# Kernel tuning notes

Measured on AMD Instinct MI355X. Metric: run time of the kernel, lower is better.

The kernel has to match this reference:

```python
import jax, jax.numpy as jnp
import numpy as np

N = 50000
E = 800000
IN_DIM = 128
HID = 64
HEADS = 4

def _gat_layer(h, src, dst, W, al, ar, Wres, activation):
    # h: [N, F_in]; W: [F_in, HEADS*HID]; al/ar: [HEADS, HID]
    n = h.shape[0]
    ft = (h @ W).reshape(n, HEADS, HID)                    # [N,H,D]
    el = (ft * al).sum(-1)                                  # [N,H]
    er = (ft * ar).sum(-1)                                  # [N,H]
    e = jax.nn.leaky_relu(el[src] + er[dst], 0.2)           # [E,H]
    m = jax.ops.segment_max(e, dst, num_segments=n)         # per-dst max for stable softmax
    ex = jnp.exp(e - m[dst])
    den = jax.ops.segment_sum(ex, dst, num_segments=n)
    alpha = ex / den[dst]                                   # edge softmax [E,H]
    out = jax.ops.segment_sum(alpha[:, :, None] * ft[src], dst, num_segments=n)  # [N,H,D]
    res = (h @ Wres).reshape(n, HEADS, HID) if Wres is not None else h.reshape(n, HEADS, HID)
    out = out + res
    return activation(out) if activation is not None else out


def setup_inputs() -> dict:
    key = jax.random.key(0)
    ks = jax.random.split(key, 16)
    def lin(k, fi, fo):
        return jax.random.normal(k, (fi, fo), jnp.float32) / np.sqrt(fi)
    HD = HEADS * HID
    inp = {
        "h": jax.random.normal(ks[0], (N, IN_DIM), jnp.float32),
        "src": jax.random.randint(ks[1], (E,), 0, N, jnp.int32),
        "dst": jax.random.randint(ks[2], (E,), 0, N, jnp.int32),
        "W1": lin(ks[3], IN_DIM, HD),
        "Wr1": lin(ks[4], IN_DIM, HD),
        "al1": jax.random.normal(ks[5], (HEADS, HID), jnp.float32) * 0.1,
        "ar1": jax.random.normal(ks[6], (HEADS, HID), jnp.float32) * 0.1,
        "W2": lin(ks[7], HD, HD),
        "al2": jax.random.normal(ks[8], (HEADS, HID), jnp.float32) * 0.1,
        "ar2": jax.random.normal(ks[9], (HEADS, HID), jnp.float32) * 0.1,
        "W3": lin(ks[10], HD, HD),
        "al3": jax.random.normal(ks[11], (HEADS, HID), jnp.float32) * 0.1,
        "ar3": jax.random.normal(ks[12], (HEADS, HID), jnp.float32) * 0.1,
        "Wm1": lin(ks[13], HID, HID),
        "bm1": jnp.zeros((HID,), jnp.float32),
        "Wm2": lin(ks[14], HID, 1),
        "bm2": jnp.zeros((1,), jnp.float32),
    }
    return inp


def reference(h, src, dst, W1, Wr1, al1, ar1, W2, al2, ar2, W3, al3, ar3, Wm1, bm1, Wm2, bm2):
    x = _gat_layer(h, src, dst, W1, al1, ar1, Wr1, jax.nn.relu)   # [N,H,D]
    x = x.reshape(x.shape[0], -1)                                  # [N,H*D]
    x = _gat_layer(x, src, dst, W2, al2, ar2, None, jax.nn.relu)  # identity residual (in==H*D)
    x = x.reshape(x.shape[0], -1)
    x = _gat_layer(x, src, dst, W3, al3, ar3, None, None)
    hf = x.mean(1)                                                 # [N,HID]
    diff = jnp.abs(hf[src] - hf[dst])                              # [E,HID]
    z = jax.nn.relu(diff @ Wm1 + bm1)
    score = jax.nn.sigmoid(z @ Wm2 + bm2).squeeze(-1)              # [E]
    return score
```

## Files before the change

### kernel.cpp

```cpp
#include <hip/hip_runtime.h>
#include <hip/hip_bf16.h>

typedef unsigned short u16;
typedef unsigned char u8;
typedef __attribute__((ext_vector_type(8))) short bf16x8;
typedef __attribute__((ext_vector_type(4))) float f32x4;
typedef __attribute__((ext_vector_type(2))) float f32x2;

__device__ __forceinline__ float bf2f(u16 u){
  union { unsigned int i; float f; } v; v.i = ((unsigned int)u) << 16; return v.f;
}
__device__ __forceinline__ u16 f2bf(float f){
  union { float f; unsigned int i; } v; v.f = f;
  unsigned int lsb = (v.i >> 16) & 1u;
  v.i += 0x7fffu + lsb;
  return (u16)(v.i >> 16);
}
__device__ __forceinline__ unsigned pkbf(float a, float b){
  __hip_bfloat162 h = __float22bfloat162_rn(make_float2(a, b));
  union { __hip_bfloat162 h2; unsigned u; } c; c.h2 = h; return c.u;
}
__device__ __forceinline__ u8 f2fp8(float f){
  int p = __builtin_amdgcn_cvt_pk_fp8_f32(f, f, 0, false);
  return (u8)(p & 0xFF);
}

__global__ void k_sniff(const u16* __restrict__ p, int* __restrict__ flag){
  __shared__ int s[256];
  int tid = threadIdx.x;
  u16 v = p[2 * tid];
  int e = (v >> 7) & 0xFF;
  s[tid] = (e >= 100 && e <= 135) ? 1 : 0;
  __syncthreads();
  for (int off = 128; off; off >>= 1){
    if (tid < off) s[tid] += s[tid + off];
    __syncthreads();
  }
  if (tid == 0) *flag = (s[0] < 180) ? 1 : 0;
}

struct PrepEnt { const void* s; void* d; void* d2; int n; int K; int mode; int bstart; };
struct Prep16 { PrepEnt e[16]; };
__global__ void k_prep(Prep16 tab, const u16* __restrict__ hsrc){
  __shared__ int s[256];
  __shared__ u16 tl[32][33];
  {
    int tid = threadIdx.x;
    u16 v = hsrc[2 * tid];
    int e = (v >> 7) & 0xFF;
    s[tid] = (e >= 100 && e <= 135) ? 1 : 0;
    __syncthreads();
    for (int off = 128; off; off >>= 1){
      if (tid < off) s[tid] += s[tid + off];
      __syncthreads();
    }
  }
  const int flag = (s[0] < 180) ? 1 : 0;
  __syncthreads();

  const int bx = blockIdx.x;
  int y = 0;
  #pragma unroll
  for (int i = 1; i < 16; ++i) if (bx >= tab.e[i].bstart) y = i;
  PrepEnt en = tab.e[y];
  const int nblk = ((y < 15) ? tab.e[y + 1].bstart : (int)gridDim.x) - en.bstart;
  const int lb = bx - en.bstart;
  const int T = nblk * 256;
  const int t0 = lb * 256 + threadIdx.x;

  if (en.mode == 1){
    u16* d = (u16*)en.d;
    for (int i = t0; i < en.n; i += T){
      u16 o[4];
      if (flag){
        float4 v = ((const float4*)en.s)[i];
        o[0] = f2bf(v.x); o[1] = f2bf(v.y); o[2] = f2bf(v.z); o[3] = f2bf(v.w);
      } else {
        uint2 v = ((const uint2*)en.s)[i];
        o[0] = (u16)v.x; o[1] = (u16)(v.x >> 16); o[2] = (u16)v.y; o[3] = (u16)(v.y >> 16);
      }
      uint2 w; w.x = o[0] | ((unsigned)o[1] << 16); w.y = o[2] | ((unsigned)o[3] << 16);
      ((uint2*)d)[i] = w;
    }
  } else if (en.mode == 0){
    u16* d = (u16*)en.d;
    for (int i = t0; i < en.n; i += T){
      if (flag) d[i] = f2bf(((const float*)en.s)[i]);
      else      d[i] = ((const u16*)en.s)[i];
    }
  } else if (en.mode == 2){
    u16* wt = (u16*)en.d;
    const int K = en.K;
    const int tk = lb >> 3, tc = lb & 7;
    const int tx = threadIdx.x & 31, ty = threadIdx.x >> 5;
    #pragma unroll
    for (int r = 0; r < 4; ++r){
      int row = tk * 32 + ty + r * 8, col = tc * 32 + tx;
      u16 b;
      if (flag) b = f2bf(((const float*)en.s)[row * 256 + col]);
      else      b = ((const u16*)en.s)[row * 256 + col];
      tl[ty + r * 8][tx] = b;
    }
    __syncthreads();
    #pragma unroll
    for (int r = 0; r < 4; ++r){
      int c = tc * 32 + ty + r * 8, k = tk * 32 + tx;
      wt[(size_t)c * K + k] = tl[tx][ty + r * 8];
    }
  } else {
    const int* dstp = (const int*)en.s;
    int* slotp = (int*)en.d;
    int* cur   = (int*)en.d2;
    for (int base = t0; base < en.n; base += 4 * T){
      int e0 = base, e1 = base + T, e2 = base + 2 * T, e3 = base + 3 * T;
      bool v0 = e0 < en.n, v1 = e1 < en.n, v2 = e2 < en.n, v3 = e3 < en.n;
      int d0 = 0, d1 = 0, d2 = 0, d3 = 0;
      if (v0) d0 = dstp[e0];
      if (v1) d1 = dstp[e1];
      if (v2) d2 = dstp[e2];
      if (v3) d3 = dstp[e3];
      int p0 = 0, p1 = 0, p2 = 0, p3 = 0;
      if (v0) p0 = atomicAdd(&cur[d0], 1);
      if (v1) p1 = atomicAdd(&cur[d1], 1);
      if (v2) p2 = atomicAdd(&cur[d2], 1);
      if (v3) p3 = atomicAdd(&cur[d3], 1);
      if (v0) slotp[e0] = p0;
      if (v1) slotp[e1] = p1;
      if (v2) slotp[e2] = p2;
      if (v3) slotp[e3] = p3;
    }
  }
}

__global__ void k_scan1(const int* __restrict__ cnt, int* __restrict__ rowptr,
                        int* __restrict__ bsums, int N){
  __shared__ int s[256];
  int i = blockIdx.x * 256 + threadIdx.x;
  int v = (i < N) ? cnt[i] : 0;
  s[threadIdx.x] = v; __syncthreads();
  for (int off = 1; off < 256; off <<= 1){
    int x = 0;
    if (threadIdx.x >= off) x = s[threadIdx.x - off];
    __syncthreads();
    s[threadIdx.x] += x;
    __syncthreads();
  }
  if (i < N) rowptr[i + 1] = s[threadIdx.x];
  if (threadIdx.x == 255) bsums[blockIdx.x] = s[255];
}
__global__ void k_scan2(int* __restrict__ bsums, int nb){
  __shared__ int s[256];
  int t = threadIdx.x;
  int v = (t < nb) ? bsums[t] : 0;
  s[t] = v; __syncthreads();
  for (int off = 1; off < 256; off <<= 1){
    int x = 0;
    if (t >= off) x = s[t - off];
    __syncthreads();
    s[t] += x;
    __syncthreads();
  }
  if (t < nb) bsums[t] = s[t] - v;
}
__global__ void k_scan3(int* __restrict__ rowptr, const int* __restrict__ bsums, int N){
  int i = blockIdx.x * 256 + threadIdx.x;
  if (i < N){
    rowptr[i + 1] += bsums[blockIdx.x];
    if (i == 0) rowptr[0] = 0;
  }
}
__global__ void k_place(const int* __restrict__ src, const int* __restrict__ dst,
                        const int* __restrict__ slot, const int* __restrict__ rowptr,
                        int4* __restrict__ csrp, int E){
  const int T = gridDim.x * 256;
  for (int i = blockIdx.x * 256 + threadIdx.x; i < E; i += T){
    int d = dst[i];
    csrp[rowptr[d] + slot[i]] = make_int4(src[i], d, i, 0);
  }
}
__global__ void k_extract(const int4* __restrict__ csrp, int* __restrict__ csrs, int E){
  int i = blockIdx.x * 256 + threadIdx.x;
  if (i < E) csrs[i] = csrp[i].x;
}

__global__ __launch_bounds__(256, 4) void mfma_gemm_v4(
    const u16* __restrict__ X, const u16* __restrict__ WT, const u16* __restrict__ WTr,
    u8* __restrict__ FT8, u16* __restrict__ XA,
    const u16* __restrict__ al, const u16* __restrict__ ar,
    float* __restrict__ el4, float* __restrict__ er4, int N, int K)
{
  extern __shared__ u16 Bs[];
  const int wv = threadIdx.x >> 6;
  const int lane = threadIdx.x & 63;
  const int m = lane & 15;
  const int q = lane >> 4;
  const int row0 = blockIdx.x * 128 + wv * 32;
  const int col0 = blockIdx.y * 128;
  const u16* W = (blockIdx.z == 0) ? WT : WTr;

  {
    const int spr = K >> 3;
    const int ish = (spr == 32) ? 5 : 4;
    const int nIss = K >> 4;
    for (int j = 0; j < nIss; ++j){
      int cbase = (j * 4 + wv) * 64;
      int chunk = cbase + lane;
      int col = chunk >> ish;
      int slot = chunk & (spr - 1);
      int gslot = slot ^ (col & 7);
      const u16* srcp = W + (size_t)(col0 + col) * K + gslot * 8;
      u16* dstp = Bs + (size_t)cbase * 8;
      __builtin_amdgcn_global_load_lds((const unsigned int*)srcp,
                                       (unsigned int*)dstp, 16, 0, 0);
    }
  }

  f32x4 acc[2][8];
  #pragma unroll
  for (int g = 0; g < 2; ++g)
    #pragma unroll
    for (int t = 0; t < 8; ++t) acc[g][t] = (f32x4){0.f, 0.f, 0.f, 0.f};
  const int rA = row0 + m, rB = row0 + 16 + m;
  const bool vA = rA < N, vB = rB < N;
  const u16* apA = X + (size_t)rA * K + q * 8;
  const u16* apB = X + (size_t)rB * K + q * 8;

  asm volatile("s_waitcnt vmcnt(0)" ::: "memory");
  __syncthreads();

  const int mh = m & 7;
  for (int k0 = 0; k0 < K; k0 += 32){
    bf16x8 aA = {}, aB = {};
    if (vA) aA = *(const bf16x8*)(apA + k0);
    if (vB) aB = *(const bf16x8*)(apB + k0);
    const int sb = (k0 >> 3) + q;
    #pragma unroll
    for (int t = 0; t < 8; ++t){
      const u16* bp = Bs + (size_t)(t * 16 + m) * K + (size_t)(sb ^ mh) * 8;
      bf16x8 b = *(const bf16x8*)bp;
      acc[0][t] = __builtin_amdgcn_mfma_f32_16x16x32_bf16(aA, b, acc[0][t], 0, 0, 0);
      acc[1][t] = __builtin_amdgcn_mfma_f32_16x16x32_bf16(aB, b, acc[1][t], 0, 0, 0);
    }
  }

  if (blockIdx.z == 0){
    float alv[8], arv[8];
    #pragma unroll
    for (int t = 0; t < 8; ++t){
      alv[t] = bf2f(al[col0 + t * 16 + m]);
      arv[t] = bf2f(ar[col0 + t * 16 + m]);
    }
    #pragma unroll
    for (int g = 0; g < 2; ++g)
      #pragma unroll
      for (int r = 0; r < 4; ++r){
        float pe[2] = {0.f, 0.f}, pr[2] = {0.f, 0.f};
        #pragma unroll
        for (int t = 0; t < 8; ++t){
          pe[t >> 2] += acc[g][t][r] * alv[t];
          pr[t >> 2] += acc[g][t][r] * arv[t];
        }
        #pragma unroll
        for (int mk = 1; mk < 16; mk <<= 1){
          pe[0] += __shfl_xor(pe[0], mk); pe[1] += __shfl_xor(pe[1], mk);
          pr[0] += __shfl_xor(pr[0], mk); pr[1] += __shfl_xor(pr[1], mk);
        }
        int rr = row0 + g * 16 + q * 4 + r;
        if (m == 0 && rr < N){
          *(float2*)(el4 + (size_t)rr * 4 + blockIdx.y * 2) = make_float2(pe[0], pe[1]);
          *(float2*)(er4 + (size_t)rr * 4 + blockIdx.y * 2) = make_float2(pr[0], pr[1]);
        }
      }
    #pragma unroll
    for (int g = 0; g < 2; ++g)
      #pragma unroll
      for (int t = 0; t < 8; ++t){
        int col = col0 + t * 16 + m;
        #pragma unroll
        for (int r = 0; r < 4; ++r){
          int rr = row0 + g * 16 + q * 4 + r;
          if (rr < N) FT8[(size_t)rr * 256 + col] = f2fp8(acc[g][t][r]);
        }
      }
  } else {
    #pragma unroll
    for (int g = 0; g < 2; ++g)
      #pragma unroll
      for (int t = 0; t < 8; ++t){
        int col = col0 + t * 16 + m;
        #pragma unroll
        for (int r = 0; r < 4; ++r){
          int rr = row0 + g * 16 + q * 4 + r;
          if (rr < N) XA[(size_t)rr * 256 + col] = f2bf(acc[g][t][r]);
        }
      }
  }
}

__global__ __launch_bounds__(256) void aggregate7(
    const u8* __restrict__ ft8, const float* __restrict__ el4, const float* __restrict__ er4,
    const int* __restrict__ rowptr, const int* __restrict__ csrs,
    const u16* __restrict__ residb, u16* __restrict__ outb,
    u16* __restrict__ hf, int do_hf, int N)
{
  __shared__ float sal[4][64][4];
  __shared__ int   sof[4][64];
  const int w = threadIdx.x >> 6, lane = threadIdx.x & 63;
  const int d = blockIdx.x * 4 + w;
  if (d >= N) return;
  const int beg = rowptr[d], deg = rowptr[d + 1] - beg;
  const int H = lane >> 5;
  const int c = lane & 31;
  const int hg = c >> 3;
  f32x2 acc2[4];
  #pragma unroll
  for (int i = 0; i < 4; ++i) acc2[i] = (f32x2){0.f, 0.f};

  if (deg > 0){
    const float4 erd = ((const float4*)er4)[d];
    const int dc = min(deg, 64);
    float x0 = 0.f, x1 = 0.f, x2 = 0.f, x3 = 0.f; int sc = 0;
    float d0 = 0.f, d1 = 0.f, d2 = 0.f, d3 = 0.f;
    for (int j = lane; j < deg; j += 64){
      int s = csrs[beg + j];
      float4 ql = ((const float4*)el4)[s];
      float e0 = ql.x + erd.x; e0 = (e0 > 0.f) ? e0 : 0.2f * e0;
      float e1 = ql.y + erd.y; e1 = (e1 > 0.f) ? e1 : 0.2f * e1;
      float e2 = ql.z + erd.z; e2 = (e2 > 0.f) ? e2 : 0.2f * e2;
      float e3 = ql.w + erd.w; e3 = (e3 > 0.f) ? e3 : 0.2f * e3;
      float t0 = __expf(fminf(e0, 60.f)), t1 = __expf(fminf(e1, 60.f));
      float t2 = __expf(fminf(e2, 60.f)), t3 = __expf(fminf(e3, 60.f));
      if (j < 64){ x0 = t0; x1 = t1; x2 = t2; x3 = t3; sc = s; }
      d0 += t0; d1 += t1; d2 += t2; d3 += t3;
    }
    for (int mk = 1; mk < dc; mk <<= 1){
      d0 += __shfl_xor(d0, mk); d1 += __shfl_xor(d1, mk);
      d2 += __shfl_xor(d2, mk); d3 += __shfl_xor(d3, mk);
    }
    const float i0 = 1.f / d0, i1 = 1.f / d1, i2 = 1.f / d2, i3 = 1.f / d3;

    for (int c0 = 0; c0 < deg; c0 += 64){
      int cs = min(64, deg - c0);
      if (lane < cs){
        float t0, t1, t2, t3; int s;
        if (c0 == 0){ t0 = x0; t1 = x1; t2 = x2; t3 = x3; s = sc; }
        else {
          s = csrs[beg + c0 + lane];
          float4 ql = ((const float4*)el4)[s];
          float e0 = ql.x + erd.x; e0 = (e0 > 0.f) ? e0 : 0.2f * e0;
          float e1 = ql.y + erd.y; e1 = (e1 > 0.f) ? e1 : 0.2f * e1;
          float e2 = ql.z + erd.z; e2 = (e2 > 0.f) ? e2 : 0.2f * e2;
          float e3 = ql.w + erd.w; e3 = (e3 > 0.f) ? e3 : 0.2f * e3;
          t0 = __expf(fminf(e0, 60.f)); t1 = __expf(fminf(e1, 60.f));
          t2 = __expf(fminf(e2, 60.f)); t3 = __expf(fminf(e3, 60.f));
        }
        sal[w][lane][0] = t0 * i0; sal[w][lane][1] = t1 * i1;
        sal[w][lane][2] = t2 * i2; sal[w][lane][3] = t3 * i3;
        sof[w][lane] = s << 8;
      }
      __builtin_amdgcn_wave_barrier();
      for (int j0 = 0; j0 < cs; j0 += 4){
        int jA = j0 + H, jB = j0 + 2 + H;
        bool bA = jA < cs, bB = jB < cs;
        float aA = 0.f, aB = 0.f;
        int offA = 0, offB = 0;
        if (bA){ aA = sal[w][jA][hg]; offA = sof[w][jA]; }
        if (bB){ aB = sal[w][jB][hg]; offB = sof[w][jB]; }
        uint2 vA = {}, vB = {};
        if (bA) vA = *(const uint2*)(ft8 + (size_t)(unsigned)offA + c * 8);
        if (bB) vB = *(const uint2*)(ft8 + (size_t)(unsigned)offB + c * 8);
        if (bA){
          f32x2 a2 = (f32x2){aA, aA};
          acc2[0] += __builtin_amdgcn_cvt_pk_f32_fp8(vA.x, 0) * a2;
          acc2[1] += __builtin_amdgcn_cvt_pk_f32_fp8(vA.x, 1) * a2;
          acc2[2] += __builtin_amdgcn_cvt_pk_f32_fp8(vA.y, 0) * a2;
          acc2[3] += __builtin_amdgcn_cvt_pk_f32_fp8(vA.y, 1) * a2;
        }
        if (bB){
          f32x2 a2 = (f32x2){aB, aB};
          acc2[0] += __builtin_amdgcn_cvt_pk_f32_fp8(vB.x, 0) * a2;
          acc2[1] += __builtin_amdgcn_cvt_pk_f32_fp8(vB.x, 1) * a2;
          acc2[2] += __builtin_amdgcn_cvt_pk_f32_fp8(vB.y, 0) * a2;
          acc2[3] += __builtin_amdgcn_cvt_pk_f32_fp8(vB.y, 1) * a2;
        }
      }
      __builtin_amdgcn_wave_barrier();
    }
  }
  float acc[8];
  #pragma unroll
  for (int i = 0; i < 4; ++i){ acc[2 * i] = acc2[i].x; acc[2 * i + 1] = acc2[i].y; }
  #pragma unroll
  for (int i = 0; i < 8; ++i) acc[i] += __shfl_xor(acc[i], 32);
  uint4 rv = *(const uint4*)(residb + (size_t)d * 256 + c * 8);
  float rr[8];
  {
    union { unsigned u; float f; } t;
    t.u = rv.x << 16; rr[0] = t.f; t.u = rv.x & 0xffff0000u; rr[1] = t.f;
    t.u = rv.y << 16; rr[2] = t.f; t.u = rv.y & 0xffff0000u; rr[3] = t.f;
    t.u = rv.z << 16; rr[4] = t.f; t.u = rv.z & 0xffff0000u; rr[5] = t.f;
    t.u = rv.w << 16; rr[6] = t.f; t.u = rv.w & 0xffff0000u; rr[7] = t.f;
  }
  if (!do_hf){
    if (H == 0){
      float o[8];
      #pragma unroll
      for (int i = 0; i < 8; ++i) o[i] = fmaxf(acc[i] + rr[i], 0.f);
      uint4 ov;
      ov.x = pkbf(o[0], o[1]); ov.y = pkbf(o[2], o[3]);
      ov.z = pkbf(o[4], o[5]); ov.w = pkbf(o[6], o[7]);
      *(uint4*)(outb + (size_t)d * 256 + c * 8) = ov;
    }
  } else {
    #pragma unroll
    for (int i = 0; i < 8; ++i){
      float o = acc[i] + rr[i];
      o += __shfl_xor(o, 8);
      o += __shfl_xor(o, 16);
      acc[i] = 0.25f * o;
    }
    if (lane < 8){
      uint4 ov;
      ov.x = pkbf(acc[0], acc[1]); ov.y = pkbf(acc[2], acc[3]);
      ov.z = pkbf(acc[4], acc[5]); ov.w = pkbf(acc[6], acc[7]);
      *(uint4*)(hf + (size_t)d * 64 + lane * 8) = ov;
    }
  }
}

__global__ __launch_bounds__(256) void edge_mlp_csr(
    const u16* __restrict__ hfb, const int4* __restrict__ csrp,
    const u16* __restrict__ Wm1, const u16* __restrict__ bm1,
    const u16* __restrict__ Wm2, const u16* __restrict__ bm2,
    void* __restrict__ out, int E, const int* __restrict__ flag)
{
  const int lane = threadIdx.x & 63;
  const int m = lane & 15;
  const int q = lane >> 4;
  const int is_f32 = *flag;

  bf16x8 bfr[4][2];
  #pragma unroll
  for (int t = 0; t < 4; ++t)
    #pragma unroll
    for (int ks = 0; ks < 2; ++ks)
      #pragma unroll
      for (int j = 0; j < 8; ++j)
        bfr[t][ks][j] = (short)Wm1[(size_t)(ks * 32 + q * 8 + j) * 64 + t * 16 + m];

  float b1v[4], w2v[4];
  #pragma unroll
  for (int t = 0; t < 4; ++t){
    b1v[t] = bf2f(bm1[t * 16 + m]);
    w2v[t] = bf2f(Wm2[t * 16 + m]);
  }
  const float b2 = bf2f(bm2[0]);

  const int wid = blockIdx.x * 4 + (threadIdx.x >> 6);
  const int nw  = gridDim.x * 4;
  for (int e0 = wid * 16; e0 < E; e0 += nw * 16){
    int e = e0 + m; if (e >= E) e = E - 1;
    int4 ed = csrp[e];
    const u16* ps = hfb + (size_t)ed.x * 64;
    const u16* pd = hfb + (size_t)ed.y * 64;
    union { bf16x8 v; uint4 u; } af[2];
    #pragma unroll
    for (int ks = 0; ks < 2; ++ks){
      bf16x8 vs = *(const bf16x8*)(ps + ks * 32 + q * 8);
      bf16x8 vd = *(const bf16x8*)(pd + ks * 32 + q * 8);
      unsigned pk[4];
      #pragma unroll
      for (int pp = 0; pp < 4; ++pp){
        float a0 = fabsf(bf2f((u16)vs[2 * pp])     - bf2f((u16)vd[2 * pp]));
        float a1 = fabsf(bf2f((u16)vs[2 * pp + 1]) - bf2f((u16)vd[2 * pp + 1]));
        pk[pp] = pkbf(a0, a1);
      }
      af[ks].u = make_uint4(pk[0], pk[1], pk[2], pk[3]);
    }
    f32x4 acc[4];
    #pragma unroll
    for (int t = 0; t < 4; ++t) acc[t] = (f32x4){0.f, 0.f, 0.f, 0.f};
    #pragma unroll
    for (int ks = 0; ks < 2; ++ks)
      #pragma unroll
      for (int t = 0; t < 4; ++t)
        acc[t] = __builtin_amdgcn_mfma_f32_16x16x32_bf16(af[ks].v, bfr[t][ks], acc[t], 0, 0, 0);
    #pragma unroll
    for (int r = 0; r < 4; ++r){
      float p = 0.f;
      #pragma unroll
      for (int t = 0; t < 4; ++t)
        p += fmaxf(acc[t][r] + b1v[t], 0.f) * w2v[t];
      #pragma unroll
      for (int mm = 1; mm < 16; mm <<= 1) p += __shfl_xor(p, mm);
      int slot = e0 + q * 4 + r;
      if (m == 0 && slot < E){
        int eid = csrp[slot].z;
        float sc = 1.f / (1.f + __expf(-(p + b2)));
        if (is_f32) ((float*)out)[eid] = sc;
        else        ((u16*)out)[eid]   = f2bf(sc);
      }
    }
  }
}

extern "C" void kernel_launch(void* const* d_in, const int* in_sizes, int n_in,
                              void* d_out, int out_size, void* d_ws, size_t ws_size,
                              hipStream_t stream)
{
  const int* src = (const int*)d_in[1];
  const int* dst = (const int*)d_in[2];

  const int N = in_sizes[0] / 128;
  const int E = in_sizes[1];

  char* p = (char*)d_ws;
  auto alloc = [&](size_t bytes) -> char* {
    char* r = p; p += (bytes + 255) & ~(size_t)255; return r;
  };
  int* flag   = (int*)  alloc(4);
  u16* hc     = (u16*)  alloc((size_t)N * 128 * 2);
  u8*  FT8    = (u8*)   alloc((size_t)N * 256);
  u16* XA     = (u16*)  alloc((size_t)N * 256 * 2);
  u16* XB     = (u16*)  alloc((size_t)N * 256 * 2);
  float* el   = (float*)alloc((size_t)N * 4 * 4);
  float* er   = (float*)alloc((size_t)N * 4 * 4);
  u16* hfb    = (u16*)  alloc((size_t)N * 64 * 2);
  int* rowptr = (int*)  alloc((size_t)(N + 1) * 4);
  int* cursor = (int*)  alloc((size_t)N * 4);
  int* slot   = (int*)  alloc((size_t)E * 4);
  int4* csrp  = (int4*) alloc((size_t)E * 16);
  int* csrs   = (int*)  alloc((size_t)E * 4);
  int* bsums  = (int*)  alloc(1024);
  u16* WT1    = (u16*)  alloc(128 * 256 * 2);
  u16* WTr1   = (u16*)  alloc(128 * 256 * 2);
  u16* WT2    = (u16*)  alloc(256 * 256 * 2);
  u16* WT3    = (u16*)  alloc(256 * 256 * 2);
  u16* al1c   = (u16*)  alloc(256 * 2);
  u16* ar1c   = (u16*)  alloc(256 * 2);
  u16* al2c   = (u16*)  alloc(256 * 2);
  u16* ar2c   = (u16*)  alloc(256 * 2);
  u16* al3c   = (u16*)  alloc(256 * 2);
  u16* ar3c   = (u16*)  alloc(256 * 2);
  u16* Wm1c   = (u16*)  alloc(4096 * 2);
  u16* bm1c   = (u16*)  alloc(64 * 2);
  u16* Wm2c   = (u16*)  alloc(64 * 2);
  u16* bm2c   = (u16*)  alloc(2);

  const int nb = (N + 255) / 256;
  const int ge = (E + 255) / 256;
  const u16* hsrc = (const u16*)d_in[0];

  k_sniff<<<1, 256, 0, stream>>>(hsrc, flag);
  hipMemsetAsync(cursor, 0, (size_t)N * 4, stream);

  {
    Prep16 t{};
    int b = 0;
    auto put = [&](int idx, const void* s, void* d, void* d2, int n, int K,
                   int mode, int nblk){
      t.e[idx] = {s, d, d2, n, K, mode, b};
      b += nblk;
    };
    put(0,  dst,      slot,  cursor, E,         0,   4, 1024);
    put(1,  d_in[0],  hc,    nullptr, N * 32,   0,   1, 768);
    put(2,  d_in[3],  WT1,   nullptr, 0,        128, 2, 32);
    put(3,  d_in[4],  WTr1,  nullptr, 0,        128, 2, 32);
    put(4,  d_in[7],  WT2,   nullptr, 0,        256, 2, 64);
    put(5,  d_in[10], WT3,   nullptr, 0,        256, 2, 64);
    put(6,  d_in[5],  al1c,  nullptr, 256,      0,   0, 1);
    put(7,  d_in[6],  ar1c,  nullptr, 256,      0,   0, 1);
    put(8,  d_in[8],  al2c,  nullptr, 256,      0,   0, 1);
    put(9,  d_in[9],  ar2c,  nullptr, 256,      0,   0, 1);
    put(10, d_in[11], al3c,  nullptr, 256,      0,   0, 1);
    put(11, d_in[12], ar3c,  nullptr, 256,      0,   0, 1);
    put(12, d_in[13], Wm1c,  nullptr, 4096,     0,   0, 1);
    put(13, d_in[14], bm1c,  nullptr, 64,       0,   0, 1);
    put(14, d_in[15], Wm2c,  nullptr, 64,       0,   0, 1);
    put(15, d_in[16], bm2c,  nullptr, 1,        0,   0, 1);
    k_prep<<<dim3(b), 256, 0, stream>>>(t, hsrc);
  }

  k_scan1<<<nb, 256, 0, stream>>>(cursor, rowptr, bsums, N);
  k_scan2<<<1, 256, 0, stream>>>(bsums, nb);
  k_scan3<<<nb, 256, 0, stream>>>(rowptr, bsums, N);
  k_place<<<512, 256, 0, stream>>>(src, dst, slot, rowptr, csrp, E);
  k_extract<<<ge, 256, 0, stream>>>(csrp, csrs, E);

  const dim3 gA3((N + 127) / 128, 2);
  const dim3 gL1((N + 127) / 128, 2, 2);
  const int gG = (N + 3) / 4;
  const int lds1 = 128 * 128 * 2;
  const int lds2 = 128 * 256 * 2;
  mfma_gemm_v4<<<gL1, 256, lds1, stream>>>(hc, WT1, WTr1, FT8, XA, al1c, ar1c, el, er, N, 128);
  aggregate7<<<gG, 256, 0, stream>>>(FT8, el, er, rowptr, csrs, XA, XB, nullptr, 0, N);
  mfma_gemm_v4<<<gA3, 256, lds2, stream>>>(XB, WT2, WT2, FT8, XA, al2c, ar2c, el, er, N, 256);
  aggregate7<<<gG, 256, 0, stream>>>(FT8, el, er, rowptr, csrs, XB, XA, nullptr, 0, N);
  mfma_gemm_v4<<<gA3, 256, lds2, stream>>>(XA, WT3, WT3, FT8, XB, al3c, ar3c, el, er, N, 256);
  aggregate7<<<gG, 256, 0, stream>>>(FT8, el, er, rowptr, csrs, XA, nullptr, hfb, 1, N);
  edge_mlp_csr<<<2048, 256, 0, stream>>>(hfb, csrp, Wm1c, bm1c, Wm2c, bm2c,
                                         d_out, E, flag);
}
```

Measured before the change: 419.7 us.

## Process four destination nodes per wave with one-pass softmax in aggregation

```diff
diff --git a/kernel.cpp b/kernel.cpp
--- a/kernel.cpp
+++ b/kernel.cpp
@@ -297,133 +297,134 @@
   }
 }
 
-__global__ __launch_bounds__(256) void aggregate7(
+__global__ __launch_bounds__(256) void aggregate8(
     const u8* __restrict__ ft8, const float* __restrict__ el4, const float* __restrict__ er4,
     const int* __restrict__ rowptr, const int* __restrict__ csrs,
     const u16* __restrict__ residb, u16* __restrict__ outb,
     u16* __restrict__ hf, int do_hf, int N)
 {
-  __shared__ float sal[4][64][4];
-  __shared__ int   sof[4][64];
+  __shared__ float sal[4][4][17][4];
+  __shared__ int   sof[4][4][16];
   const int w = threadIdx.x >> 6, lane = threadIdx.x & 63;
-  const int d = blockIdx.x * 4 + w;
-  if (d >= N) return;
-  const int beg = rowptr[d], deg = rowptr[d + 1] - beg;
-  const int H = lane >> 5;
-  const int c = lane & 31;
-  const int hg = c >> 3;
-  f32x2 acc2[4];
+  const int g = lane >> 4, t = lane & 15;
+  const int hd = t >> 2;
+  const int d = blockIdx.x * 16 + w * 4 + g;
+  const bool vd = d < N;
+  int beg = 0, deg = 0;
+  if (vd){ beg = rowptr[d]; deg = rowptr[d + 1] - beg; }
+  int mdeg = deg;
+  mdeg = max(mdeg, __shfl_xor(mdeg, 16));
+  mdeg = max(mdeg, __shfl_xor(mdeg, 32));
+  float4 erd = make_float4(0.f, 0.f, 0.f, 0.f);
+  if (vd) erd = ((const float4*)er4)[d];
+
+  f32x2 acc2[8];
   #pragma unroll
-  for (int i = 0; i < 4; ++i) acc2[i] = (f32x2){0.f, 0.f};
-
-  if (deg > 0){
-    const float4 erd = ((const float4*)er4)[d];
-    const int dc = min(deg, 64);
-    float x0 = 0.f, x1 = 0.f, x2 = 0.f, x3 = 0.f; int sc = 0;
-    float d0 = 0.f, d1 = 0.f, d2 = 0.f, d3 = 0.f;
-    for (int j = lane; j < deg; j += 64){
-      int s = csrs[beg + j];
+  for (int i = 0; i < 8; ++i) acc2[i] = (f32x2){0.f, 0.f};
+  float den[4] = {0.f, 0.f, 0.f, 0.f};
+
+  for (int c0 = 0; c0 < mdeg; c0 += 16){
+    const int rem = deg - c0;
+    float t0 = 0.f, t1 = 0.f, t2 = 0.f, t3 = 0.f; int s = 0;
+    if (t < rem){
+      s = csrs[beg + c0 + t];
       float4 ql = ((const float4*)el4)[s];
       float e0 = ql.x + erd.x; e0 = (e0 > 0.f) ? e0 : 0.2f * e0;
       float e1 = ql.y + erd.y; e1 = (e1 > 0.f) ? e1 : 0.2f * e1;
       float e2 = ql.z + erd.z; e2 = (e2 > 0.f) ? e2 : 0.2f * e2;
       float e3 = ql.w + erd.w; e3 = (e3 > 0.f) ? e3 : 0.2f * e3;
-      float t0 = __expf(fminf(e0, 60.f)), t1 = __expf(fminf(e1, 60.f));
-      float t2 = __expf(fminf(e2, 60.f)), t3 = __expf(fminf(e3, 60.f));
-      if (j < 64){ x0 = t0; x1 = t1; x2 = t2; x3 = t3; sc = s; }
-      d0 += t0; d1 += t1; d2 += t2; d3 += t3;
-    }
-    for (int mk = 1; mk < dc; mk <<= 1){
-      d0 += __shfl_xor(d0, mk); d1 += __shfl_xor(d1, mk);
-      d2 += __shfl_xor(d2, mk); d3 += __shfl_xor(d3, mk);
-    }
-    const float i0 = 1.f / d0, i1 = 1.f / d1, i2 = 1.f / d2, i3 = 1.f / d3;
-
-    for (int c0 = 0; c0 < deg; c0 += 64){
-      int cs = min(64, deg - c0);
-      if (lane < cs){
-        float t0, t1, t2, t3; int s;
-        if (c0 == 0){ t0 = x0; t1 = x1; t2 = x2; t3 = x3; s = sc; }
-        else {
-          s = csrs[beg + c0 + lane];
-          float4 ql = ((const float4*)el4)[s];
-          float e0 = ql.x + erd.x; e0 = (e0 > 0.f) ? e0 : 0.2f * e0;
-          float e1 = ql.y + erd.y; e1 = (e1 > 0.f) ? e1 : 0.2f * e1;
-          float e2 = ql.z + erd.z; e2 = (e2 > 0.f) ? e2 : 0.2f * e2;
-          float e3 = ql.w + erd.w; e3 = (e3 > 0.f) ? e3 : 0.2f * e3;
-          t0 = __expf(fminf(e0, 60.f)); t1 = __expf(fminf(e1, 60.f));
-          t2 = __expf(fminf(e2, 60.f)); t3 = __expf(fminf(e3, 60.f));
-        }
-        sal[w][lane][0] = t0 * i0; sal[w][lane][1] = t1 * i1;
-        sal[w][lane][2] = t2 * i2; sal[w][lane][3] = t3 * i3;
-        sof[w][lane] = s << 8;
-      }
-      __builtin_amdgcn_wave_barrier();
-      for (int j0 = 0; j0 < cs; j0 += 4){
-        int jA = j0 + H, jB = j0 + 2 + H;
-        bool bA = jA < cs, bB = jB < cs;
-        float aA = 0.f, aB = 0.f;
-        int offA = 0, offB = 0;
-        if (bA){ aA = sal[w][jA][hg]; offA = sof[w][jA]; }
-        if (bB){ aB = sal[w][jB][hg]; offB = sof[w][jB]; }
-        uint2 vA = {}, vB = {};
-        if (bA) vA = *(const uint2*)(ft8 + (size_t)(unsigned)offA + c * 8);
-        if (bB) vB = *(const uint2*)(ft8 + (size_t)(unsigned)offB + c * 8);
-        if (bA){
-          f32x2 a2 = (f32x2){aA, aA};
-          acc2[0] += __builtin_amdgcn_cvt_pk_f32_fp8(vA.x, 0) * a2;
-          acc2[1] += __builtin_amdgcn_cvt_pk_f32_fp8(vA.x, 1) * a2;
-          acc2[2] += __builtin_amdgcn_cvt_pk_f32_fp8(vA.y, 0) * a2;
-          acc2[3] += __builtin_amdgcn_cvt_pk_f32_fp8(vA.y, 1) * a2;
-        }
-        if (bB){
-          f32x2 a2 = (f32x2){aB, aB};
-          acc2[0] += __builtin_amdgcn_cvt_pk_f32_fp8(vB.x, 0) * a2;
-          acc2[1] += __builtin_amdgcn_cvt_pk_f32_fp8(vB.x, 1) * a2;
-          acc2[2] += __builtin_amdgcn_cvt_pk_f32_fp8(vB.y, 0) * a2;
-          acc2[3] += __builtin_amdgcn_cvt_pk_f32_fp8(vB.y, 1) * a2;
-        }
-      }
-      __builtin_amdgcn_wave_barrier();
-    }
-  }
-  float acc[8];
+      t0 = __expf(fminf(e0, 60.f)); t1 = __expf(fminf(e1, 60.f));
+      t2 = __expf(fminf(e2, 60.f)); t3 = __expf(fminf(e3, 60.f));
+    }
+    den[0] += t0; den[1] += t1; den[2] += t2; den[3] += t3;
+    sal[w][g][t][0] = t0; sal[w][g][t][1] = t1;
+    sal[w][g][t][2] = t2; sal[w][g][t][3] = t3;
+    sof[w][g][t] = s << 8;
+    __builtin_amdgcn_wave_barrier();
+    int cr = rem < 16 ? (rem < 0 ? 0 : rem) : 16;
+    int jm = (cr + 3) & ~3;
+    for (int j = 0; j < jm; j += 4){
+      float a[4]; unsigned off[4]; uint4 v[4];
+      #pragma unroll
+      for (int u = 0; u < 4; ++u){
+        a[u] = sal[w][g][j + u][hd];
+        off[u] = (unsigned)sof[w][g][j + u];
+      }
+      #pragma unroll
+      for (int u = 0; u < 4; ++u)
+        v[u] = *(const uint4*)(ft8 + (size_t)off[u] + t * 16);
+      #pragma unroll
+      for (int u = 0; u < 4; ++u){
+        f32x2 a2 = (f32x2){a[u], a[u]};
+        acc2[0] += __builtin_amdgcn_cvt_pk_f32_fp8(v[u].x, 0) * a2;
+        acc2[1] += __builtin_amdgcn_cvt_pk_f32_fp8(v[u].x, 1) * a2;
+        acc2[2] += __builtin_amdgcn_cvt_pk_f32_fp8(v[u].y, 0) * a2;
+        acc2[3] += __builtin_amdgcn_cvt_pk_f32_fp8(v[u].y, 1) * a2;
+        acc2[4] += __builtin_amdgcn_cvt_pk_f32_fp8(v[u].z, 0) * a2;
+        acc2[5] += __builtin_amdgcn_cvt_pk_f32_fp8(v[u].z, 1) * a2;
+        acc2[6] += __builtin_amdgcn_cvt_pk_f32_fp8(v[u].w, 0) * a2;
+        acc2[7] += __builtin_amdgcn_cvt_pk_f32_fp8(v[u].w, 1) * a2;
+      }
+    }
+    __builtin_amdgcn_wave_barrier();
+  }
   #pragma unroll
-  for (int i = 0; i < 4; ++i){ acc[2 * i] = acc2[i].x; acc[2 * i + 1] = acc2[i].y; }
+  for (int mk = 1; mk < 16; mk <<= 1){
+    den[0] += __shfl_xor(den[0], mk); den[1] += __shfl_xor(den[1], mk);
+    den[2] += __shfl_xor(den[2], mk); den[3] += __shfl_xor(den[3], mk);
+  }
+  const float dh = den[hd];
+  const float inv = (dh > 0.f) ? (1.f / dh) : 0.f;
+
+  if (!vd) return;
+  const u16* rp = residb + (size_t)d * 256 + t * 16;
+  uint4 r0 = *(const uint4*)rp;
+  uint4 r1 = *(const uint4*)(rp + 8);
+  float o[16];
+  {
+    union { unsigned u; float f; } x;
+    unsigned rw[8] = {r0.x, r0.y, r0.z, r0.w, r1.x, r1.y, r1.z, r1.w};
+    #pragma unroll
+    for (int i = 0; i < 8; ++i){
+      x.u = rw[i] << 16;          o[2 * i]     = x.f;
+      x.u = rw[i] & 0xffff0000u;  o[2 * i + 1] = x.f;
+    }
+  }
   #pragma unroll
-  for (int i = 0; i < 8; ++i) acc[i] += __shfl_xor(acc[i], 32);
-  uint4 rv = *(const uint4*)(residb + (size_t)d * 256 + c * 8);
-  float rr[8];
-  {
-    union { unsigned u; float f; } t;
-    t.u = rv.x << 16; rr[0] = t.f; t.u = rv.x & 0xffff0000u; rr[1] = t.f;
-    t.u = rv.y << 16; rr[2] = t.f; t.u = rv.y & 0xffff0000u; rr[3] = t.f;
-    t.u = rv.z << 16; rr[4] = t.f; t.u = rv.z & 0xffff0000u; rr[5] = t.f;
-    t.u = rv.w << 16; rr[6] = t.f; t.u = rv.w & 0xffff0000u; rr[7] = t.f;
+  for (int i = 0; i < 8; ++i){
+    o[2 * i]     += acc2[i].x * inv;
+    o[2 * i + 1] += acc2[i].y * inv;
   }
   if (!do_hf){
-    if (H == 0){
-      float o[8];
-      #pragma unroll
-      for (int i = 0; i < 8; ++i) o[i] = fmaxf(acc[i] + rr[i], 0.f);
-      uint4 ov;
-      ov.x = pkbf(o[0], o[1]); ov.y = pkbf(o[2], o[3]);
-      ov.z = pkbf(o[4], o[5]); ov.w = pkbf(o[6], o[7]);
-      *(uint4*)(outb + (size_t)d * 256 + c * 8) = ov;
-    }
+    uint4 a, b;
+    a.x = pkbf(fmaxf(o[0], 0.f),  fmaxf(o[1], 0.f));
+    a.y = pkbf(fmaxf(o[2], 0.f),  fmaxf(o[3], 0.f));
+    a.z = pkbf(fmaxf(o[4], 0.f),  fmaxf(o[5], 0.f));
+    a.w = pkbf(fmaxf(o[6], 0.f),  fmaxf(o[7], 0.f));
+    b.x = pkbf(fmaxf(o[8], 0.f),  fmaxf(o[9], 0.f));
+    b.y = pkbf(fmaxf(o[10], 0.f), fmaxf(o[11], 0.f));
+    b.z = pkbf(fmaxf(o[12], 0.f), fmaxf(o[13], 0.f));
+    b.w = pkbf(fmaxf(o[14], 0.f), fmaxf(o[15], 0.f));
+    u16* op = outb + (size_t)d * 256 + t * 16;
+    *(uint4*)op = a;
+    *(uint4*)(op + 8) = b;
   } else {
     #pragma unroll
-    for (int i = 0; i < 8; ++i){
-      float o = acc[i] + rr[i];
-      o += __shfl_xor(o, 8);
-      o += __shfl_xor(o, 16);
-      acc[i] = 0.25f * o;
-    }
-    if (lane < 8){
-      uint4 ov;
-      ov.x = pkbf(acc[0], acc[1]); ov.y = pkbf(acc[2], acc[3]);
-      ov.z = pkbf(acc[4], acc[5]); ov.w = pkbf(acc[6], acc[7]);
-      *(uint4*)(hf + (size_t)d * 64 + lane * 8) = ov;
+    for (int i = 0; i < 16; ++i){
+      float v = o[i];
+      v += __shfl_xor(v, 4);
+      v += __shfl_xor(v, 8);
+      o[i] = 0.25f * v;
+    }
+    if (t < 4){
+      uint4 a, b;
+      a.x = pkbf(o[0], o[1]);   a.y = pkbf(o[2], o[3]);
+      a.z = pkbf(o[4], o[5]);   a.w = pkbf(o[6], o[7]);
+      b.x = pkbf(o[8], o[9]);   b.y = pkbf(o[10], o[11]);
+      b.z = pkbf(o[12], o[13]); b.w = pkbf(o[14], o[15]);
+      u16* hp = hf + (size_t)d * 64 + t * 16;
+      *(uint4*)hp = a;
+      *(uint4*)(hp + 8) = b;
     }
   }
 }
@@ -589,15 +590,15 @@
 
   const dim3 gA3((N + 127) / 128, 2);
   const dim3 gL1((N + 127) / 128, 2, 2);
-  const int gG = (N + 3) / 4;
+  const int gG = (N + 15) / 16;
   const int lds1 = 128 * 128 * 2;
   const int lds2 = 128 * 256 * 2;
   mfma_gemm_v4<<<gL1, 256, lds1, stream>>>(hc, WT1, WTr1, FT8, XA, al1c, ar1c, el, er, N, 128);
-  aggregate7<<<gG, 256, 0, stream>>>(FT8, el, er, rowptr, csrs, XA, XB, nullptr, 0, N);
+  aggregate8<<<gG, 256, 0, stream>>>(FT8, el, er, rowptr, csrs, XA, XB, nullptr, 0, N);
   mfma_gemm_v4<<<gA3, 256, lds2, stream>>>(XB, WT2, WT2, FT8, XA, al2c, ar2c, el, er, N, 256);
-  aggregate7<<<gG, 256, 0, stream>>>(FT8, el, er, rowptr, csrs, XB, XA, nullptr, 0, N);
+  aggregate8<<<gG, 256, 0, stream>>>(FT8, el, er, rowptr, csrs, XB, XA, nullptr, 0, N);
   mfma_gemm_v4<<<gA3, 256, lds2, stream>>>(XA, WT3, WT3, FT8, XB, al3c, ar3c, el, er, N, 256);
-  aggregate7<<<gG, 256, 0, stream>>>(FT8, el, er, rowptr, csrs, XA, nullptr, hfb, 1, N);
+  aggregate8<<<gG, 256, 0, stream>>>(FT8, el, er, rowptr, csrs, XA, nullptr, hfb, 1, N);
   edge_mlp_csr<<<2048, 256, 0, stream>>>(hfb, csrp, Wm1c, bm1c, Wm2c, bm2c,
                                          d_out, E, flag);
 }
```

Measured after the change: 402.5 us. 4.1% less time.
